# Kernel optimization log

Hardware: AMD Instinct MI355X
Metric: run time of the kernel (lower is better)

Reference implementation:

```python
import jax, jax.numpy as jnp
import numpy as np

B, T, D, H, V, K = 64, 128, 300, 256, 30000, 16
FILTERS = [3, 4, 5]
FN = [100, 100, 100]
CLS = 5


def setup_inputs() -> dict:
    key = jax.random.key(0)
    ks = jax.random.split(key, 32)
    n = lambda i, shape, s=0.05: (jax.random.normal(ks[i], shape, jnp.float32) * s)
    inp = jax.random.randint(ks[0], (B, T), 0, V)
    emb = n(1, (V + 2, D)).at[V + 1].set(0.0)  # padding_idx row = 0
    # GRU (1 layer, bidirectional), PyTorch gate order r,z,n
    Wx_f, Wh_f = n(2, (3 * H, D)), n(3, (3 * H, H))
    bx_f, bh_f = n(4, (3 * H,)), n(5, (3 * H,))
    Wx_b, Wh_b = n(6, (3 * H, D)), n(7, (3 * H, H))
    bx_b, bh_b = n(8, (3 * H,)), n(9, (3 * H,))
    fc1c_W, fc1c_b = n(10, (D, 2 * H)), n(11, (D,))
    concept_table = n(12, (V, K, D), 0.1)
    counts = jax.random.randint(ks[13], (V,), 1, K + 1)
    concept_mask = (jnp.arange(K)[None, :] < counts[:, None])  # bool [V,K]
    conv_W0, conv_b0 = n(14, (FN[0], FILTERS[0] * 2 * D)), n(15, (FN[0],))
    conv_W1, conv_b1 = n(16, (FN[1], FILTERS[1] * 2 * D)), n(17, (FN[1],))
    conv_W2, conv_b2 = n(18, (FN[2], FILTERS[2] * 2 * D)), n(19, (FN[2],))
    fc1_W, fc1_b = n(20, (100, sum(FN))), n(21, (100,))
    fc2_W, fc2_b = n(22, (CLS, 100)), n(23, (CLS,))
    return dict(inp=inp, emb=emb, Wx_f=Wx_f, Wh_f=Wh_f, bx_f=bx_f, bh_f=bh_f,
                Wx_b=Wx_b, Wh_b=Wh_b, bx_b=bx_b, bh_b=bh_b,
                fc1c_W=fc1c_W, fc1c_b=fc1c_b,
                concept_table=concept_table, concept_mask=concept_mask,
                conv_W0=conv_W0, conv_b0=conv_b0, conv_W1=conv_W1, conv_b1=conv_b1,
                conv_W2=conv_W2, conv_b2=conv_b2,
                fc1_W=fc1_W, fc1_b=fc1_b, fc2_W=fc2_W, fc2_b=fc2_b)


def _gru_dir(x, Wx, Wh, bx, bh):
    # x: [B,T,D] -> hidden states [B,T,H]; PyTorch GRU cell math.
    xg = jnp.einsum('btd,gd->btg', x, Wx) + bx  # precompute input gates [B,T,3H]

    def step(h, xg_t):
        gh = h @ Wh.T + bh
        xr, xz, xn = jnp.split(xg_t, 3, axis=-1)
        hr, hz, hn = jnp.split(gh, 3, axis=-1)
        r = jax.nn.sigmoid(xr + hr)
        z = jax.nn.sigmoid(xz + hz)
        nn_ = jnp.tanh(xn + r * hn)
        h2 = (1.0 - z) * nn_ + z * h
        return h2, h2

    h0 = jnp.zeros((x.shape[0], Wh.shape[1]), x.dtype)
    _, ys = jax.lax.scan(step, h0, jnp.swapaxes(xg, 0, 1))
    return jnp.swapaxes(ys, 0, 1)


def _forward(inp, emb, Wx_f, Wh_f, bx_f, bh_f, Wx_b, Wh_b, bx_b, bh_b,
             fc1c_W, fc1c_b, concept_table, concept_mask,
             conv_W0, conv_b0, conv_W1, conv_b1, conv_W2, conv_b2,
             fc1_W, fc1_b, fc2_W, fc2_b):
    x = emb[inp]                                   # [B,T,D]
    hf = _gru_dir(x, Wx_f, Wh_f, bx_f, bh_f)
    hb = jnp.flip(_gru_dir(jnp.flip(x, 1), Wx_b, Wh_b, bx_b, bh_b), 1)
    out = jnp.concatenate([hf, hb], axis=-1)       # [B,T,2H]
    ctx = jnp.einsum('bth,dh->btd', out, fc1c_W) + fc1c_b  # [B,T,D] context
    # batched gather-attend-reduce over per-word concept lists
    conc = concept_table[inp]                      # [B,T,K,D]
    mask = concept_mask[inp]                       # [B,T,K] bool
    scores = jnp.einsum('btkd,btd->btk', conc, ctx)
    scores = jnp.where(mask, scores, jnp.float32(-1e30))
    attn = jax.nn.softmax(scores, axis=-1)
    concept = jnp.einsum('btk,btkd->btd', attn, conc)
    concept = jax.lax.stop_gradient(concept)       # original detaches via .data.numpy()
    feat = jnp.concatenate([ctx, concept], axis=-1)  # [B,T,2D]
    pooled = []
    for fs, W, b in ((FILTERS[0], conv_W0, conv_b0),
                     (FILTERS[1], conv_W1, conv_b1),
                     (FILTERS[2], conv_W2, conv_b2)):
        L = T - fs + 1
        # Conv1d(kernel=2D*fs, stride=2D) over flattened feat == token-window matmul
        win = jnp.concatenate([feat[:, i:i + L, :] for i in range(fs)], axis=-1)  # [B,L,fs*2D]
        c = jax.nn.relu(jnp.einsum('blk,fk->blf', win, W) + b)
        pooled.append(jnp.max(c, axis=1))          # max-pool over positions -> [B,FN]
    h = jnp.concatenate(pooled, axis=1)            # [B,300]; dropout is identity in eval
    h = h @ fc1_W.T + fc1_b
    h = h @ fc2_W.T + fc2_b
    return jax.nn.softmax(h, axis=1)


def reference(inp, emb, Wx_f, Wh_f, bx_f, bh_f, Wx_b, Wh_b, bx_b, bh_b,
              fc1c_W, fc1c_b, concept_table, concept_mask,
              conv_W0, conv_b0, conv_W1, conv_b1, conv_W2, conv_b2,
              fc1_W, fc1_b, fc2_W, fc2_b):
    return _forward(inp, emb, Wx_f, Wh_f, bx_f, bh_f, Wx_b, Wh_b, bx_b, bh_b,
                    fc1c_W, fc1c_b, concept_table, concept_mask,
                    conv_W0, conv_b0, conv_W1, conv_b1, conv_W2, conv_b2,
                    fc1_W, fc1_b, fc2_W, fc2_b)
```

## Files before the change

kernel.cpp:

```cpp
#include <hip/hip_runtime.h>


typedef unsigned short u16;
typedef unsigned int u32;
typedef __attribute__((ext_vector_type(4))) u16 u16x4;
typedef __attribute__((ext_vector_type(8))) u16 u16x8;
typedef __attribute__((ext_vector_type(8))) __bf16 bf16x8;
typedef __attribute__((ext_vector_type(4))) float f32x4;

__device__ __forceinline__ float bf2f(u16 u) {
    union { u32 i; float f; } x; x.i = ((u32)u) << 16; return x.f;
}
__device__ __forceinline__ u16 f2bf(float f) {
    union { float f; u32 i; } x; x.f = f;
    u32 r = x.i + 0x7FFFu + ((x.i >> 16) & 1u);
    return (u16)(r >> 16);
}
__device__ __forceinline__ float sigm(float x) { return 1.f / (1.f + __expf(-x)); }
__device__ __forceinline__ float tanh_(float x) {
    float e = __expf(-2.f * fabsf(x));
    float t = (1.f - e) / (1.f + e);
    return x < 0.f ? -t : t;
}
__device__ __forceinline__ void gload16(const u16* g, u16* l) {
    __builtin_amdgcn_global_load_lds(
        (const __attribute__((address_space(1))) void*)g,
        (__attribute__((address_space(3))) void*)l, 16, 0, 0);
}

__global__ __launch_bounds__(256) void detect_k(
    const u32* __restrict__ cmask_raw, int* __restrict__ flags)
{
    __shared__ int cnt1;
    if (threadIdx.x == 0) cnt1 = 0;
    __syncthreads();
    int c1 = 0;
    for (int i = threadIdx.x; i < 1024; i += 256)
        if (cmask_raw[i] > 1u) c1++;
    if (c1) atomicAdd(&cnt1, c1);
    __syncthreads();
    if (threadIdx.x == 0) flags[1] = (cnt1 > 0) ? 1 : 0;
}

struct CvtDesc { const void* src; u16* dst; int n; };
struct CvtArgs { CvtDesc d[11]; };

__global__ __launch_bounds__(256) void convert_f32(CvtArgs a)
{
    CvtDesc de = a.d[blockIdx.y];
    int i4 = (blockIdx.x * 256 + threadIdx.x) * 4;
    if (i4 >= de.n) return;
    const float* s = (const float*)de.src + i4;
    if (i4 + 4 <= de.n) {
        u16x4 o; o[0] = f2bf(s[0]); o[1] = f2bf(s[1]); o[2] = f2bf(s[2]); o[3] = f2bf(s[3]);
        *(u16x4*)(de.dst + i4) = o;
    } else {
        for (int e = 0; e < 4 && i4 + e < de.n; ++e) de.dst[i4 + e] = f2bf(s[e]);
    }
}

__global__ __launch_bounds__(256) void build_mask(
    const void* __restrict__ cmask, int* __restrict__ mask16, const int* __restrict__ flags)
{
    int v = blockIdx.x * 256 + threadIdx.x;
    if (v >= 30000) return;
    int m = 0;
    if (flags[1]) {
        const unsigned char* p = (const unsigned char*)cmask + (size_t)v * 16;
#pragma unroll
        for (int k = 0; k < 16; ++k) if (p[k]) m |= (1 << k);
    } else {
        const int* p = (const int*)cmask + (size_t)v * 16;
#pragma unroll
        for (int k = 0; k < 16; ++k) if (p[k]) m |= (1 << k);
    }
    mask16[v] = m;
}

__global__ __launch_bounds__(256) void repack_conv(
    const float* __restrict__ cw0, const float* __restrict__ cw1,
    const float* __restrict__ cw2, u16* __restrict__ wcat)
{
    const int r = blockIdx.x;
    const int d0 = threadIdx.x * 4;
    if (d0 >= 640) return;
    u16x4 o = {0, 0, 0, 0};
    if (r < 1200 && d0 < 600) {
        const float* src;
        if (r < 300)      { int f = r % 100,       i = r / 100;          src = cw0 + (size_t)f * 1800 + i * 600; }
        else if (r < 700) { int rr = r - 300, f = rr % 100, i = rr / 100; src = cw1 + (size_t)f * 2400 + i * 600; }
        else              { int rr = r - 700, f = rr % 100, i = rr / 100; src = cw2 + (size_t)f * 3000 + i * 600; }
        float4 x = *(const float4*)(src + d0);
        o[0] = f2bf(x.x); o[1] = f2bf(x.y); o[2] = f2bf(x.z); o[3] = f2bf(x.w);
    }
    *(u16x4*)(wcat + (size_t)r * 640 + d0) = o;
}

__global__ __launch_bounds__(64) void pack_wx(
    const float* __restrict__ wxf, const float* __restrict__ wxb,
    u16* __restrict__ wxpad)
{
    const int n = blockIdx.x;
    const float* src = n < 768 ? wxf + (size_t)n * 300 : wxb + (size_t)(n - 768) * 300;
    for (int c = threadIdx.x; c < 80; c += 64) {
        u16x4 o = {0, 0, 0, 0};
        if (c < 75) {
            float4 x = *(const float4*)(src + c * 4);
            o[0] = f2bf(x.x); o[1] = f2bf(x.y); o[2] = f2bf(x.z); o[3] = f2bf(x.w);
        }
        *(u16x4*)(wxpad + (size_t)n * 320 + c * 4) = o;
    }
}

__global__ __launch_bounds__(256) void build_bias(
    const float* __restrict__ bxf, const float* __restrict__ bhf,
    const float* __restrict__ bxb, const float* __restrict__ bhb,
    float* __restrict__ bias2)
{
    int c = blockIdx.x * 256 + threadIdx.x;
    if (c >= 1536) return;
    int cc = c < 768 ? c : c - 768;
    const float* bx = c < 768 ? bxf : bxb;
    const float* bh = c < 768 ? bhf : bhb;
    float v = bx[cc];
    if (cc < 512) v += bh[cc];
    bias2[c] = v;
}

__global__ __launch_bounds__(64) void stage_x(
    const int* __restrict__ inp, const float* __restrict__ emb,
    u16* __restrict__ xstage)
{
    const int tok = blockIdx.x;
    const float* src = emb + (size_t)inp[tok] * 300;
    for (int c = threadIdx.x; c < 80; c += 64) {
        u16x4 o = {0, 0, 0, 0};
        if (c < 75) {
            float4 x = *(const float4*)(src + c * 4);
            o[0] = f2bf(x.x); o[1] = f2bf(x.y); o[2] = f2bf(x.z); o[3] = f2bf(x.w);
        }
        *(u16x4*)(xstage + (size_t)tok * 320 + c * 4) = o;
    }
}

template<int EPI>
__global__ __launch_bounds__(256) void gemm128(
    const u16* __restrict__ A, const u16* __restrict__ W,
    const float* __restrict__ bias, u16* __restrict__ C,
    int Kpad, int Nout, int ldc)
{
    __shared__ __align__(16) u16 sA[128 * 32];
    __shared__ __align__(16) u16 sW[128 * 32];

    const int tid = threadIdx.x;
    const int n0 = blockIdx.x * 128;
    const int m0 = blockIdx.y * 128;

    const int l  = tid & 63;
    const int w  = tid >> 6;
    const int wm = (w >> 1) << 6;
    const int wn = (w & 1) << 6;
    const int fr = l & 15;
    const int fk = (l >> 4) << 3;

    const int srow = tid >> 2;
    const int scol = (tid & 3) << 3;

    f32x4 acc[4][4];
#pragma unroll
    for (int i = 0; i < 4; ++i)
#pragma unroll
        for (int j = 0; j < 4; ++j) acc[i][j] = (f32x4){0.f, 0.f, 0.f, 0.f};

    for (int k0 = 0; k0 < Kpad; k0 += 32) {
        __syncthreads();
#pragma unroll
        for (int i = 0; i < 2; ++i) {
            gload16(A + (size_t)(m0 + i * 64 + srow) * Kpad + k0 + scol,
                    sA + i * 2048 + tid * 8);
            gload16(W + (size_t)(n0 + i * 64 + srow) * Kpad + k0 + scol,
                    sW + i * 2048 + tid * 8);
        }
        __syncthreads();

        bf16x8 a[4], b[4];
#pragma unroll
        for (int i = 0; i < 4; ++i) {
            a[i] = *(const bf16x8*)(sA + (wm + i * 16 + fr) * 32 + fk);
            b[i] = *(const bf16x8*)(sW + (wn + i * 16 + fr) * 32 + fk);
        }
#pragma unroll
        for (int i = 0; i < 4; ++i)
#pragma unroll
            for (int j = 0; j < 4; ++j)
                acc[i][j] = __builtin_amdgcn_mfma_f32_16x16x32_bf16(a[i], b[j], acc[i][j], 0, 0, 0);
    }

    const int rb = (l >> 4) << 2;
    const int cc = l & 15;
#pragma unroll
    for (int j = 0; j < 4; ++j) {
        const int col = n0 + wn + j * 16 + cc;
        if (col < Nout) {
            const float bv = (EPI == 1) ? bias[col] : 0.f;
#pragma unroll
            for (int i = 0; i < 4; ++i) {
#pragma unroll
                for (int r = 0; r < 4; ++r) {
                    const int row = m0 + wm + i * 16 + rb + r;
                    C[(size_t)row * ldc + col] = f2bf(acc[i][j][r] + bv);
                }
            }
        }
    }
}

__global__ __launch_bounds__(256) void gemm_bt(
    const u16* __restrict__ A, const u16* __restrict__ W,
    const u16* __restrict__ bias, u16* __restrict__ Cb,
    int M, int N, int K, int lda, int ldc)
{
    __shared__ __align__(16) u16 sA[64 * 40];
    __shared__ __align__(16) u16 sW[64 * 40];

    const int tid = threadIdx.x;
    const int m0 = blockIdx.y * 64;
    const int n0 = blockIdx.x * 64;

    const int l  = tid & 63;
    const int w  = tid >> 6;
    const int wm = (w >> 1) << 5;
    const int wn = (w & 1) << 5;
    const int fr = l & 15;
    const int fk = (l >> 4) << 3;

    const int sr = tid >> 2;
    const int cb = (tid & 3) << 3;

    const size_t abase = (size_t)(m0 + sr) * (size_t)lda;
    const int  wrow   = n0 + sr;
    const bool wvalid = wrow < N;
    const size_t wbase = (size_t)wrow * (size_t)K;

    f32x4 acc00 = {0,0,0,0}, acc01 = {0,0,0,0}, acc10 = {0,0,0,0}, acc11 = {0,0,0,0};

    for (int k0 = 0; k0 < K; k0 += 32) {
        __syncthreads();
        {
            const u16* p = A + abase + k0 + cb;
            *(u16x4*)(sA + sr * 40 + cb)     = *(const u16x4*)p;
            *(u16x4*)(sA + sr * 40 + cb + 4) = *(const u16x4*)(p + 4);
        }
        {
            u16x4 v0 = {0,0,0,0}, v1 = {0,0,0,0};
            if (wvalid) {
                const u16* p = W + wbase + k0 + cb;
                v0 = *(const u16x4*)p;
                v1 = *(const u16x4*)(p + 4);
            }
            *(u16x4*)(sW + sr * 40 + cb)     = v0;
            *(u16x4*)(sW + sr * 40 + cb + 4) = v1;
        }
        __syncthreads();

        bf16x8 a0 = *(const bf16x8*)(sA + (wm + fr)      * 40 + fk);
        bf16x8 a1 = *(const bf16x8*)(sA + (wm + 16 + fr) * 40 + fk);
        bf16x8 b0 = *(const bf16x8*)(sW + (wn + fr)      * 40 + fk);
        bf16x8 b1 = *(const bf16x8*)(sW + (wn + 16 + fr) * 40 + fk);

        acc00 = __builtin_amdgcn_mfma_f32_16x16x32_bf16(a0, b0, acc00, 0, 0, 0);
        acc01 = __builtin_amdgcn_mfma_f32_16x16x32_bf16(a0, b1, acc01, 0, 0, 0);
        acc10 = __builtin_amdgcn_mfma_f32_16x16x32_bf16(a1, b0, acc10, 0, 0, 0);
        acc11 = __builtin_amdgcn_mfma_f32_16x16x32_bf16(a1, b1, acc11, 0, 0, 0);
    }

    const int rb = (l >> 4) << 2;
    const int cc = l & 15;
#define EPILOG(ACC, I, J)                                                     \
    {                                                                         \
        int col = n0 + wn + (J)*16 + cc;                                      \
        if (col < N) {                                                        \
            float bv = bf2f(bias[col]);                                       \
            _Pragma("unroll")                                                 \
            for (int r = 0; r < 4; ++r) {                                     \
                int row = m0 + wm + (I)*16 + rb + r;                          \
                if (row < M)                                                  \
                    Cb[(size_t)row * ldc + col] = f2bf(ACC[r] + bv);          \
            }                                                                 \
        }                                                                     \
    }
    EPILOG(acc00, 0, 0); EPILOG(acc01, 0, 1); EPILOG(acc10, 1, 0); EPILOG(acc11, 1, 1);
#undef EPILOG
}

#define GB 8
__global__ __attribute__((amdgpu_waves_per_eu(2, 2)))
__launch_bounds__(512, 2) void gru_scan_mfma(
    const u16* __restrict__ xg,
    const u16* __restrict__ whf, const u16* __restrict__ whb,
    const float* __restrict__ bhf, const float* __restrict__ bhb,
    u16* __restrict__ outb)
{
    const int bg  = blockIdx.x;
    const int dir = blockIdx.y;
    const u16* wh = dir ? whb : whf;
    const float* bh = dir ? bhb : bhf;

    const int tid = threadIdx.x;
    const int w = tid >> 6;
    const int l = tid & 63;

    __shared__ __align__(16) u16 h_bf[16][264];
    __shared__ __align__(16) float gh[GB][772];

    for (int i = tid; i < 16 * 264; i += 512) ((u16*)h_bf)[i] = 0;

    bf16x8 bfr[6][8];
#pragma unroll
    for (int c = 0; c < 6; ++c)
#pragma unroll
        for (int kt = 0; kt < 8; ++kt) {
            const int n = w * 96 + c * 16 + (l & 15);
            const int k = kt * 32 + (l >> 4) * 8;
            bfr[c][kt] = *(const bf16x8*)(wh + (size_t)n * 256 + k);
        }
#pragma unroll
    for (int c = 0; c < 6; ++c)
#pragma unroll
        for (int kt = 0; kt < 8; ++kt)
            asm volatile("" : "+v"(bfr[c][kt]));

    const int qrow = (l >> 4) << 2;
    const int arow = l & 15;
    const int aofs = (l >> 4) << 3;
    const int j0 = l * 4;
    const int bglob = bg * GB + w;
    const float4 bhn4 = *(const float4*)(bh + 512 + j0);
    f32x4 hreg = {0.f, 0.f, 0.f, 0.f};

    __syncthreads();

    for (int s = 0; s < 128; ++s) {
        const int t = dir ? (127 - s) : s;

        f32x4 acc[6];
#pragma unroll
        for (int c = 0; c < 6; ++c) acc[c] = (f32x4){0.f, 0.f, 0.f, 0.f};
#pragma unroll
        for (int kt = 0; kt < 8; ++kt) {
            bf16x8 a = *(const bf16x8*)(&h_bf[arow][kt * 32 + aofs]);
#pragma unroll
            for (int c = 0; c < 6; ++c)
                acc[c] = __builtin_amdgcn_mfma_f32_16x16x32_bf16(a, bfr[c][kt], acc[c], 0, 0, 0);
        }

        const size_t tb = (size_t)(bglob * 128 + t) * 1536 + dir * 768;
        u16x4 xr4 = *(const u16x4*)(xg + tb + j0);
        u16x4 xz4 = *(const u16x4*)(xg + tb + 256 + j0);
        u16x4 xn4 = *(const u16x4*)(xg + tb + 512 + j0);

        if (qrow < GB) {
#pragma unroll
            for (int c = 0; c < 6; ++c) {
                const int col = w * 96 + c * 16 + (l & 15);
#pragma unroll
                for (int r = 0; r < 4; ++r)
                    gh[qrow + r][col] = acc[c][r];
            }
        }
        __syncthreads();

        u16x4 ho;
#pragma unroll
        for (int e = 0; e < 4; ++e) {
            const int j = j0 + e;
            float r = sigm(bf2f(xr4[e]) + gh[w][j]);
            float z = sigm(bf2f(xz4[e]) + gh[w][256 + j]);
            float n = tanh_(bf2f(xn4[e]) + r * (gh[w][512 + j] + bhn4[e]));
            float h2 = (1.f - z) * n + z * hreg[e];
            hreg[e] = h2;
            ho[e] = f2bf(h2);
        }
        *(u16x4*)(&h_bf[w][j0]) = ho;
        *(u16x4*)(outb + (size_t)(bglob * 128 + t) * 512 + dir * 256 + j0) = ho;
        __syncthreads();
    }
}
#undef GB

__global__ __launch_bounds__(256) void attn_kernel(
    const int* __restrict__ inp, const float* __restrict__ ctab,
    const int* __restrict__ mask16, u16* __restrict__ feat)
{
    const int tok = blockIdx.x;
    const int tid = threadIdx.x;
    const int v = inp[tok];

    __shared__ float ctx_s[300];
    __shared__ __align__(16) u16 conc_s[16 * 300];
    __shared__ float sc_s[16];
    __shared__ float at_s[16];

    for (int d = tid; d < 300; d += 256) ctx_s[d] = bf2f(feat[(size_t)tok * 640 + d]);
    {
        const float4* src = (const float4*)(ctab + (size_t)v * 4800);
        for (int i = tid; i < 1200; i += 256) {
            float4 x = src[i];
            u16x4 o; o[0] = f2bf(x.x); o[1] = f2bf(x.y); o[2] = f2bf(x.z); o[3] = f2bf(x.w);
            *(u16x4*)(conc_s + i * 4) = o;
        }
    }
    __syncthreads();

    const int g = tid >> 4, ln = tid & 15;
    float s = 0.f;
    for (int d = ln; d < 300; d += 16) s += bf2f(conc_s[g * 300 + d]) * ctx_s[d];
    s += __shfl_xor(s, 1); s += __shfl_xor(s, 2); s += __shfl_xor(s, 4); s += __shfl_xor(s, 8);
    if (ln == 0) sc_s[g] = ((mask16[v] >> g) & 1) ? s : -1e30f;
    __syncthreads();

    if (tid == 0) {
        float m = -1e30f;
#pragma unroll
        for (int i = 0; i < 16; ++i) m = fmaxf(m, sc_s[i]);
        float p[16]; float den = 0.f;
#pragma unroll
        for (int i = 0; i < 16; ++i) {
            float pe = (sc_s[i] <= -1e29f) ? 0.f : __expf(sc_s[i] - m);
            p[i] = pe; den += pe;
        }
        float inv = den > 0.f ? 1.f / den : 0.f;
#pragma unroll
        for (int i = 0; i < 16; ++i) at_s[i] = p[i] * inv;
    }
    __syncthreads();

    for (int d = tid; d < 340; d += 256) {
        float a = 0.f;
        if (d < 300) {
#pragma unroll
            for (int g2 = 0; g2 < 16; ++g2) a += at_s[g2] * bf2f(conc_s[g2 * 300 + d]);
        }
        feat[(size_t)tok * 640 + 300 + d] = f2bf(a);
    }
}

__global__ __launch_bounds__(128) void pool_fused(
    const u16* __restrict__ P, const u16* __restrict__ cbcat,
    float* __restrict__ pool)
{
    const int b = blockIdx.x, which = blockIdx.y, f = threadIdx.x;
    if (f >= 100) return;
    const int fs  = which == 0 ? 3 : (which == 1 ? 4 : 5);
    const int off = which == 0 ? 0 : (which == 1 ? 300 : 700);
    const int L   = 128 - fs + 1;
    const float bias = bf2f(cbcat[which * 100 + f]);
    float mm = -1e30f;
    for (int l2 = 0; l2 < L; ++l2) {
        float s = bias;
#pragma unroll 5
        for (int i = 0; i < fs; ++i)
            s += bf2f(P[(size_t)(b * 128 + l2 + i) * 1200 + off + i * 100 + f]);
        mm = fmaxf(mm, s);
    }
    pool[b * 300 + which * 100 + f] = fmaxf(mm, 0.f);
}

__global__ __launch_bounds__(128) void final_k(
    const float* __restrict__ pool,
    const u16* __restrict__ fc1W, const u16* __restrict__ fc1b,
    const u16* __restrict__ fc2W, const u16* __restrict__ fc2b,
    float* __restrict__ out)
{
    const int b = blockIdx.x, tid = threadIdx.x;
    __shared__ float ps[300], h1[100], lg[5];
    for (int d = tid; d < 300; d += 128) ps[d] = pool[b * 300 + d];
    __syncthreads();
    if (tid < 100) {
        float a = bf2f(fc1b[tid]);
        for (int k = 0; k < 300; ++k) a += bf2f(fc1W[tid * 300 + k]) * ps[k];
        h1[tid] = a;
    }
    __syncthreads();
    if (tid < 5) {
        float a = bf2f(fc2b[tid]);
        for (int k = 0; k < 100; ++k) a += bf2f(fc2W[tid * 100 + k]) * h1[k];
        lg[tid] = a;
    }
    __syncthreads();
    if (tid == 0) {
        float m = fmaxf(fmaxf(fmaxf(lg[0], lg[1]), fmaxf(lg[2], lg[3])), lg[4]);
        float e0 = __expf(lg[0] - m), e1 = __expf(lg[1] - m), e2 = __expf(lg[2] - m),
              e3 = __expf(lg[3] - m), e4 = __expf(lg[4] - m);
        float inv = 1.f / (e0 + e1 + e2 + e3 + e4);
        out[b * 5 + 0] = e0 * inv;
        out[b * 5 + 1] = e1 * inv;
        out[b * 5 + 2] = e2 * inv;
        out[b * 5 + 3] = e3 * inv;
        out[b * 5 + 4] = e4 * inv;
    }
}

extern "C" void kernel_launch(void* const* d_in, const int* in_sizes, int n_in,
                              void* d_out, int out_size, void* d_ws, size_t ws_size,
                              hipStream_t stream)
{
    (void)in_sizes; (void)n_in; (void)out_size; (void)ws_size;

    const int*  inp     = (const int*)d_in[0];
    const void* embR    = d_in[1];
    const void* WxfR    = d_in[2];
    const void* WhfR    = d_in[3];
    const void* bxfR    = d_in[4];
    const void* bhfR    = d_in[5];
    const void* WxbR    = d_in[6];
    const void* WhbR    = d_in[7];
    const void* bxbR    = d_in[8];
    const void* bhbR    = d_in[9];
    const void* fc1cWR  = d_in[10];
    const void* fc1cbR  = d_in[11];
    const void* ctabR   = d_in[12];
    const void* cmaskR  = d_in[13];
    const void* cw0R    = d_in[14];
    const void* cb0R    = d_in[15];
    const void* cw1R    = d_in[16];
    const void* cb1R    = d_in[17];
    const void* cw2R    = d_in[18];
    const void* cb2R    = d_in[19];
    const void* fc1WR   = d_in[20];
    const void* fc1bR   = d_in[21];
    const void* fc2WR   = d_in[22];
    const void* fc2bR   = d_in[23];

    char* ws = (char*)d_ws;
    size_t off = 0;
    auto alloc = [&](size_t bytes) -> char* {
        char* r = ws + off;
        off = (off + bytes + 255) & ~(size_t)255;
        return r;
    };

    u16*   xgc    = (u16*)alloc(8192ull * 1536 * 2);
    u16*   outb   = (u16*)alloc(8192ull * 512 * 2);
    u16*   feat   = (u16*)alloc(8192ull * 640 * 2);
    u16*   P      = (u16*)alloc(8192ull * 1200 * 2);
    u16*   xstage = (u16*)alloc(8192ull * 320 * 2);
    float* pool   = (float*)alloc(64ull * 300 * 4);
    int*   flags  = (int*)alloc(256);
    int*   mask16 = (int*)alloc(30000ull * 4);
    u16*   wxpad  = (u16*)alloc(1536ull * 320 * 2);
    float* bias2  = (float*)alloc(1536ull * 4);
    u16*   whfc   = (u16*)alloc(196608ull * 2);
    u16*   whbc   = (u16*)alloc(196608ull * 2);
    u16*   fc1cWc = (u16*)alloc(153600ull * 2);
    u16*   fc1cbc = (u16*)alloc(300ull * 2);
    u16*   wcat   = (u16*)alloc(1280ull * 640 * 2);
    u16*   cbcat  = (u16*)alloc(300ull * 2);
    u16*   fc1Wc  = (u16*)alloc(30000ull * 2);
    u16*   fc1bc  = (u16*)alloc(100ull * 2);
    u16*   fc2Wc  = (u16*)alloc(500ull * 2);
    u16*   fc2bc  = (u16*)alloc(8ull * 2);

    detect_k<<<1, 256, 0, stream>>>((const u32*)cmaskR, flags);

    {
        CvtArgs a{};
        a.d[0]  = { WhfR,   whfc,        196608 };
        a.d[1]  = { WhbR,   whbc,        196608 };
        a.d[2]  = { fc1cWR, fc1cWc,      153600 };
        a.d[3]  = { fc1cbR, fc1cbc,      300 };
        a.d[4]  = { cb0R,   cbcat,       100 };
        a.d[5]  = { cb1R,   cbcat + 100, 100 };
        a.d[6]  = { cb2R,   cbcat + 200, 100 };
        a.d[7]  = { fc1WR,  fc1Wc,       30000 };
        a.d[8]  = { fc1bR,  fc1bc,       100 };
        a.d[9]  = { fc2WR,  fc2Wc,       500 };
        a.d[10] = { fc2bR,  fc2bc,       5 };
        convert_f32<<<dim3(192, 11), 256, 0, stream>>>(a);
    }

    build_mask<<<118, 256, 0, stream>>>(cmaskR, mask16, flags);
    repack_conv<<<1280, 256, 0, stream>>>(
        (const float*)cw0R, (const float*)cw1R, (const float*)cw2R, wcat);
    pack_wx<<<1536, 64, 0, stream>>>((const float*)WxfR, (const float*)WxbR, wxpad);
    build_bias<<<6, 256, 0, stream>>>((const float*)bxfR, (const float*)bhfR,
                                      (const float*)bxbR, (const float*)bhbR, bias2);
    stage_x<<<8192, 64, 0, stream>>>(inp, (const float*)embR, xstage);

    gemm128<1><<<dim3(12, 64), 256, 0, stream>>>(
        xstage, wxpad, bias2, xgc, 320, 1536, 1536);

    gru_scan_mfma<<<dim3(8, 2), 512, 0, stream>>>(
        xgc, whfc, whbc, (const float*)bhfR, (const float*)bhbR, outb);

    gemm_bt<<<dim3(5, 128), 256, 0, stream>>>(
        outb, fc1cWc, fc1cbc, feat, 8192, 300, 512, 512, 640);

    attn_kernel<<<dim3(8192), 256, 0, stream>>>(inp, (const float*)ctabR, mask16, feat);

    gemm128<0><<<dim3(10, 64), 256, 0, stream>>>(
        feat, wcat, nullptr, P, 640, 1200, 1200);

    pool_fused<<<dim3(64, 3), 128, 0, stream>>>(P, cbcat, pool);

    final_k<<<dim3(64), 128, 0, stream>>>(pool, fc1Wc, fc1bc, fc2Wc, fc2bc, (float*)d_out);
}
```

Before: 511.0 us.

## Replace gemm_bt with gemm128 for fc1c, batch small pack kernels, fp32 attn staging

Result: no change. 518.0 us (+1.4%).

```diff
diff --git a/kernel.cpp b/kernel.cpp
--- a/kernel.cpp
+++ b/kernel.cpp
@@ -43,7 +43,7 @@
 }
 
 struct CvtDesc { const void* src; u16* dst; int n; };
-struct CvtArgs { CvtDesc d[11]; };
+struct CvtArgs { CvtDesc d[9]; };
 
 __global__ __launch_bounds__(256) void convert_f32(CvtArgs a)
 {
@@ -81,28 +81,29 @@
     const float* __restrict__ cw0, const float* __restrict__ cw1,
     const float* __restrict__ cw2, u16* __restrict__ wcat)
 {
-    const int r = blockIdx.x;
-    const int d0 = threadIdx.x * 4;
-    if (d0 >= 640) return;
-    u16x4 o = {0, 0, 0, 0};
-    if (r < 1200 && d0 < 600) {
-        const float* src;
-        if (r < 300)      { int f = r % 100,       i = r / 100;          src = cw0 + (size_t)f * 1800 + i * 600; }
-        else if (r < 700) { int rr = r - 300, f = rr % 100, i = rr / 100; src = cw1 + (size_t)f * 2400 + i * 600; }
-        else              { int rr = r - 700, f = rr % 100, i = rr / 100; src = cw2 + (size_t)f * 3000 + i * 600; }
-        float4 x = *(const float4*)(src + d0);
-        o[0] = f2bf(x.x); o[1] = f2bf(x.y); o[2] = f2bf(x.z); o[3] = f2bf(x.w);
-    }
-    *(u16x4*)(wcat + (size_t)r * 640 + d0) = o;
-}
-
-__global__ __launch_bounds__(64) void pack_wx(
+    const int r = blockIdx.x * 8 + (threadIdx.x >> 5);
+    for (int slot = threadIdx.x & 31; slot < 160; slot += 32) {
+        const int d0 = slot * 4;
+        u16x4 o = {0, 0, 0, 0};
+        if (r < 1200 && d0 < 600) {
+            const float* src;
+            if (r < 300)      { int f = r % 100,       i = r / 100;          src = cw0 + (size_t)f * 1800 + i * 600; }
+            else if (r < 700) { int rr = r - 300, f = rr % 100, i = rr / 100; src = cw1 + (size_t)f * 2400 + i * 600; }
+            else              { int rr = r - 700, f = rr % 100, i = rr / 100; src = cw2 + (size_t)f * 3000 + i * 600; }
+            float4 x = *(const float4*)(src + d0);
+            o[0] = f2bf(x.x); o[1] = f2bf(x.y); o[2] = f2bf(x.z); o[3] = f2bf(x.w);
+        }
+        *(u16x4*)(wcat + (size_t)r * 640 + d0) = o;
+    }
+}
+
+__global__ __launch_bounds__(256) void pack_wx(
     const float* __restrict__ wxf, const float* __restrict__ wxb,
     u16* __restrict__ wxpad)
 {
-    const int n = blockIdx.x;
+    const int n = blockIdx.x * 16 + (threadIdx.x >> 4);
     const float* src = n < 768 ? wxf + (size_t)n * 300 : wxb + (size_t)(n - 768) * 300;
-    for (int c = threadIdx.x; c < 80; c += 64) {
+    for (int c = threadIdx.x & 15; c < 80; c += 16) {
         u16x4 o = {0, 0, 0, 0};
         if (c < 75) {
             float4 x = *(const float4*)(src + c * 4);
@@ -110,6 +111,19 @@
         }
         *(u16x4*)(wxpad + (size_t)n * 320 + c * 4) = o;
     }
+}
+
+__global__ __launch_bounds__(128) void pack_fc1c(
+    const float* __restrict__ w, u16* __restrict__ dst)
+{
+    const int r = blockIdx.x;
+    const int c4 = threadIdx.x * 4;
+    u16x4 o = {0, 0, 0, 0};
+    if (r < 300) {
+        float4 x = *(const float4*)(w + (size_t)r * 512 + c4);
+        o[0] = f2bf(x.x); o[1] = f2bf(x.y); o[2] = f2bf(x.z); o[3] = f2bf(x.w);
+    }
+    *(u16x4*)(dst + (size_t)r * 512 + c4) = o;
 }
 
 __global__ __launch_bounds__(256) void build_bias(
@@ -127,13 +141,13 @@
     bias2[c] = v;
 }
 
-__global__ __launch_bounds__(64) void stage_x(
+__global__ __launch_bounds__(256) void stage_x(
     const int* __restrict__ inp, const float* __restrict__ emb,
     u16* __restrict__ xstage)
 {
-    const int tok = blockIdx.x;
+    const int tok = blockIdx.x * 8 + (threadIdx.x >> 5);
     const float* src = emb + (size_t)inp[tok] * 300;
-    for (int c = threadIdx.x; c < 80; c += 64) {
+    for (int c = threadIdx.x & 31; c < 80; c += 32) {
         u16x4 o = {0, 0, 0, 0};
         if (c < 75) {
             float4 x = *(const float4*)(src + c * 4);
@@ -213,84 +227,6 @@
             }
         }
     }
-}
-
-__global__ __launch_bounds__(256) void gemm_bt(
-    const u16* __restrict__ A, const u16* __restrict__ W,
-    const u16* __restrict__ bias, u16* __restrict__ Cb,
-    int M, int N, int K, int lda, int ldc)
-{
-    __shared__ __align__(16) u16 sA[64 * 40];
-    __shared__ __align__(16) u16 sW[64 * 40];
-
-    const int tid = threadIdx.x;
-    const int m0 = blockIdx.y * 64;
-    const int n0 = blockIdx.x * 64;
-
-    const int l  = tid & 63;
-    const int w  = tid >> 6;
-    const int wm = (w >> 1) << 5;
-    const int wn = (w & 1) << 5;
-    const int fr = l & 15;
-    const int fk = (l >> 4) << 3;
-
-    const int sr = tid >> 2;
-    const int cb = (tid & 3) << 3;
-
-    const size_t abase = (size_t)(m0 + sr) * (size_t)lda;
-    const int  wrow   = n0 + sr;
-    const bool wvalid = wrow < N;
-    const size_t wbase = (size_t)wrow * (size_t)K;
-
-    f32x4 acc00 = {0,0,0,0}, acc01 = {0,0,0,0}, acc10 = {0,0,0,0}, acc11 = {0,0,0,0};
-
-    for (int k0 = 0; k0 < K; k0 += 32) {
-        __syncthreads();
-        {
-            const u16* p = A + abase + k0 + cb;
-            *(u16x4*)(sA + sr * 40 + cb)     = *(const u16x4*)p;
-            *(u16x4*)(sA + sr * 40 + cb + 4) = *(const u16x4*)(p + 4);
-        }
-        {
-            u16x4 v0 = {0,0,0,0}, v1 = {0,0,0,0};
-            if (wvalid) {
-                const u16* p = W + wbase + k0 + cb;
-                v0 = *(const u16x4*)p;
-                v1 = *(const u16x4*)(p + 4);
-            }
-            *(u16x4*)(sW + sr * 40 + cb)     = v0;
-            *(u16x4*)(sW + sr * 40 + cb + 4) = v1;
-        }
-        __syncthreads();
-
-        bf16x8 a0 = *(const bf16x8*)(sA + (wm + fr)      * 40 + fk);
-        bf16x8 a1 = *(const bf16x8*)(sA + (wm + 16 + fr) * 40 + fk);
-        bf16x8 b0 = *(const bf16x8*)(sW + (wn + fr)      * 40 + fk);
-        bf16x8 b1 = *(const bf16x8*)(sW + (wn + 16 + fr) * 40 + fk);
-
-        acc00 = __builtin_amdgcn_mfma_f32_16x16x32_bf16(a0, b0, acc00, 0, 0, 0);
-        acc01 = __builtin_amdgcn_mfma_f32_16x16x32_bf16(a0, b1, acc01, 0, 0, 0);
-        acc10 = __builtin_amdgcn_mfma_f32_16x16x32_bf16(a1, b0, acc10, 0, 0, 0);
-        acc11 = __builtin_amdgcn_mfma_f32_16x16x32_bf16(a1, b1, acc11, 0, 0, 0);
-    }
-
-    const int rb = (l >> 4) << 2;
-    const int cc = l & 15;
-#define EPILOG(ACC, I, J)                                                     \
-    {                                                                         \
-        int col = n0 + wn + (J)*16 + cc;                                      \
-        if (col < N) {                                                        \
-            float bv = bf2f(bias[col]);                                       \
-            _Pragma("unroll")                                                 \
-            for (int r = 0; r < 4; ++r) {                                     \
-                int row = m0 + wm + (I)*16 + rb + r;                          \
-                if (row < M)                                                  \
-                    Cb[(size_t)row * ldc + col] = f2bf(ACC[r] + bv);          \
-            }                                                                 \
-        }                                                                     \
-    }
-    EPILOG(acc00, 0, 0); EPILOG(acc01, 0, 1); EPILOG(acc10, 1, 0); EPILOG(acc11, 1, 1);
-#undef EPILOG
 }
 
 #define GB 8
@@ -397,24 +333,21 @@
     const int v = inp[tok];
 
     __shared__ float ctx_s[300];
-    __shared__ __align__(16) u16 conc_s[16 * 300];
+    __shared__ __align__(16) float conc_s[16 * 300];
     __shared__ float sc_s[16];
     __shared__ float at_s[16];
 
     for (int d = tid; d < 300; d += 256) ctx_s[d] = bf2f(feat[(size_t)tok * 640 + d]);
     {
         const float4* src = (const float4*)(ctab + (size_t)v * 4800);
-        for (int i = tid; i < 1200; i += 256) {
-            float4 x = src[i];
-            u16x4 o; o[0] = f2bf(x.x); o[1] = f2bf(x.y); o[2] = f2bf(x.z); o[3] = f2bf(x.w);
-            *(u16x4*)(conc_s + i * 4) = o;
-        }
+        for (int i = tid; i < 1200; i += 256)
+            *(float4*)(conc_s + i * 4) = src[i];
     }
     __syncthreads();
 
     const int g = tid >> 4, ln = tid & 15;
     float s = 0.f;
-    for (int d = ln; d < 300; d += 16) s += bf2f(conc_s[g * 300 + d]) * ctx_s[d];
+    for (int d = ln; d < 300; d += 16) s += conc_s[g * 300 + d] * ctx_s[d];
     s += __shfl_xor(s, 1); s += __shfl_xor(s, 2); s += __shfl_xor(s, 4); s += __shfl_xor(s, 8);
     if (ln == 0) sc_s[g] = ((mask16[v] >> g) & 1) ? s : -1e30f;
     __syncthreads();
@@ -439,7 +372,7 @@
         float a = 0.f;
         if (d < 300) {
 #pragma unroll
-            for (int g2 = 0; g2 < 16; ++g2) a += at_s[g2] * bf2f(conc_s[g2 * 300 + d]);
+            for (int g2 = 0; g2 < 16; ++g2) a += at_s[g2] * conc_s[g2 * 300 + d];
         }
         feat[(size_t)tok * 640 + 300 + d] = f2bf(a);
     }
@@ -552,8 +485,7 @@
     float* bias2  = (float*)alloc(1536ull * 4);
     u16*   whfc   = (u16*)alloc(196608ull * 2);
     u16*   whbc   = (u16*)alloc(196608ull * 2);
-    u16*   fc1cWc = (u16*)alloc(153600ull * 2);
-    u16*   fc1cbc = (u16*)alloc(300ull * 2);
+    u16*   fc1cp  = (u16*)alloc(384ull * 512 * 2);
     u16*   wcat   = (u16*)alloc(1280ull * 640 * 2);
     u16*   cbcat  = (u16*)alloc(300ull * 2);
     u16*   fc1Wc  = (u16*)alloc(30000ull * 2);
@@ -565,27 +497,26 @@
 
     {
         CvtArgs a{};
-        a.d[0]  = { WhfR,   whfc,        196608 };
-        a.d[1]  = { WhbR,   whbc,        196608 };
-        a.d[2]  = { fc1cWR, fc1cWc,      153600 };
-        a.d[3]  = { fc1cbR, fc1cbc,      300 };
-        a.d[4]  = { cb0R,   cbcat,       100 };
-        a.d[5]  = { cb1R,   cbcat + 100, 100 };
-        a.d[6]  = { cb2R,   cbcat + 200, 100 };
-        a.d[7]  = { fc1WR,  fc1Wc,       30000 };
-        a.d[8]  = { fc1bR,  fc1bc,       100 };
-        a.d[9]  = { fc2WR,  fc2Wc,       500 };
-        a.d[10] = { fc2bR,  fc2bc,       5 };
-        convert_f32<<<dim3(192, 11), 256, 0, stream>>>(a);
+        a.d[0] = { WhfR,  whfc,        196608 };
+        a.d[1] = { WhbR,  whbc,        196608 };
+        a.d[2] = { cb0R,  cbcat,       100 };
+        a.d[3] = { cb1R,  cbcat + 100, 100 };
+        a.d[4] = { cb2R,  cbcat + 200, 100 };
+        a.d[5] = { fc1WR, fc1Wc,       30000 };
+        a.d[6] = { fc1bR, fc1bc,       100 };
+        a.d[7] = { fc2WR, fc2Wc,       500 };
+        a.d[8] = { fc2bR, fc2bc,       5 };
+        convert_f32<<<dim3(192, 9), 256, 0, stream>>>(a);
     }
 
     build_mask<<<118, 256, 0, stream>>>(cmaskR, mask16, flags);
-    repack_conv<<<1280, 256, 0, stream>>>(
+    repack_conv<<<160, 256, 0, stream>>>(
         (const float*)cw0R, (const float*)cw1R, (const float*)cw2R, wcat);
-    pack_wx<<<1536, 64, 0, stream>>>((const float*)WxfR, (const float*)WxbR, wxpad);
+    pack_wx<<<96, 256, 0, stream>>>((const float*)WxfR, (const float*)WxbR, wxpad);
+    pack_fc1c<<<384, 128, 0, stream>>>((const float*)fc1cWR, fc1cp);
     build_bias<<<6, 256, 0, stream>>>((const float*)bxfR, (const float*)bhfR,
                                       (const float*)bxbR, (const float*)bhbR, bias2);
-    stage_x<<<8192, 64, 0, stream>>>(inp, (const float*)embR, xstage);
+    stage_x<<<1024, 256, 0, stream>>>(inp, (const float*)embR, xstage);
 
     gemm128<1><<<dim3(12, 64), 256, 0, stream>>>(
         xstage, wxpad, bias2, xgc, 320, 1536, 1536);
@@ -593,8 +524,8 @@
     gru_scan_mfma<<<dim3(8, 2), 512, 0, stream>>>(
         xgc, whfc, whbc, (const float*)bhfR, (const float*)bhbR, outb);
 
-    gemm_bt<<<dim3(5, 128), 256, 0, stream>>>(
-        outb, fc1cWc, fc1cbc, feat, 8192, 300, 512, 512, 640);
+    gemm128<1><<<dim3(3, 64), 256, 0, stream>>>(
+        outb, fc1cp, (const float*)fc1cbR, feat, 512, 300, 640);
 
     attn_kernel<<<dim3(8192), 256, 0, stream>>>(inp, (const float*)ctabR, mask16, feat);
 
```
